# Performance work log

Hardware: AMD Instinct MI355X
Metric: run time of the kernel (lower is better)

## Reference

```python
import jax, jax.numpy as jnp
import numpy as np

N = 500_000
EMB = 256
G = 4096


def setup_inputs() -> dict:
    key = jax.random.key(0)
    k1, k2, k3, k4, k5, k6 = jax.random.split(key, 6)
    values = jax.random.normal(k1, (N, EMB), dtype=jnp.float32)
    indices = jnp.sort(jax.random.randint(k2, (N,), 0, G, dtype=jnp.int64))
    # Linear params (torch Linear: y = x @ W.T + b); stored pre-transposed.
    lim_g = 1.0 / np.sqrt(EMB)
    gate_w = jax.random.uniform(k3, (EMB, 1), jnp.float32, -lim_g, lim_g)
    gate_b = jax.random.uniform(k4, (1,), jnp.float32, -lim_g, lim_g)
    attn_w = jax.random.uniform(k5, (EMB, EMB), jnp.float32, -lim_g, lim_g)
    attn_b = jax.random.uniform(k6, (EMB,), jnp.float32, -lim_g, lim_g)
    return {
        "values": values,
        "indices": indices,
        "num_graphs": G,
        "gate_w": gate_w,
        "gate_b": gate_b,
        "attn_w": attn_w,
        "attn_b": attn_b,
    }


def reference(values, indices, num_graphs, gate_w, gate_b, attn_w, attn_b):
    # Gate scores: [N, 1]
    s = values @ gate_w + gate_b
    # Segmented softmax over nodes grouped by graph id (numerically stable).
    seg_max = jax.ops.segment_max(s, indices, num_segments=num_graphs)  # [G, 1]
    e = jnp.exp(s - seg_max[indices])                                   # [N, 1]
    denom = jax.ops.segment_sum(e, indices, num_segments=num_graphs)   # [G, 1]
    w = e / denom[indices]                                              # [N, 1]
    # Attention projection and weighted segment sum.
    a = values @ attn_w + attn_b                                        # [N, EMB]
    out = jax.ops.segment_sum(w * a, indices, num_segments=num_graphs)  # [G, EMB]
    return out
```

## Files before the change

### kernel.cpp

```cpp
#include <hip/hip_runtime.h>
#include <math.h>

#define EMB 256

__global__ void k_bounds(const int* __restrict__ idx, int* __restrict__ seg_start,
                         int n, int g) {
    int t = blockIdx.x * blockDim.x + threadIdx.x;
    if (t > g) return;
    int lo = 0, hi = n;
    while (lo < hi) {
        int mid = (lo + hi) >> 1;
        if (idx[mid] < t) lo = mid + 1; else hi = mid;
    }
    seg_start[t] = lo;
}

__global__ void __launch_bounds__(256) k_fused(const float* __restrict__ vals,
                                               const float* __restrict__ gate_w,
                                               const float* __restrict__ gate_b,
                                               const int* __restrict__ seg_start,
                                               float* __restrict__ wvec) {
    const int g = blockIdx.x;
    const int start = seg_start[g], end = seg_start[g + 1];
    const int cnt = end - start;
    const int t = threadIdx.x;
    const int lane = t & 63, w = t >> 6;

    __shared__ float m_s[4], d_s[4];
    __shared__ float partial[4][EMB];

    if (cnt <= 0) {
        wvec[(size_t)g * EMB + t] = 0.0f;
        return;
    }

    const float4 gw = *reinterpret_cast<const float4*>(gate_w + lane * 4);
    const float  gb = gate_b[0];

    float m = -INFINITY, d = 0.0f;
    float4 acc = {0.f, 0.f, 0.f, 0.f};

    for (int j = start + w; j < end; j += 4) {
        float4 v = *reinterpret_cast<const float4*>(vals + (size_t)j * EMB + lane * 4);
        float si = v.x * gw.x + v.y * gw.y + v.z * gw.z + v.w * gw.w;
        #pragma unroll
        for (int o = 1; o < 64; o <<= 1) si += __shfl_xor(si, o);
        si += gb;
        if (si > m) {
            const float scale = expf(m - si);
            d *= scale;
            acc.x *= scale; acc.y *= scale; acc.z *= scale; acc.w *= scale;
            m = si;
        }
        const float p = expf(si - m);
        d += p;
        acc.x += p * v.x; acc.y += p * v.y; acc.z += p * v.z; acc.w += p * v.w;
    }

    if (lane == 0) m_s[w] = m;
    __syncthreads();
    const float M = fmaxf(fmaxf(m_s[0], m_s[1]), fmaxf(m_s[2], m_s[3]));
    const float f = expf(m - M);
    if (lane == 0) d_s[w] = d * f;
    acc.x *= f; acc.y *= f; acc.z *= f; acc.w *= f;
    *reinterpret_cast<float4*>(&partial[w][lane * 4]) = acc;
    __syncthreads();
    const float dt = d_s[0] + d_s[1] + d_s[2] + d_s[3];
    wvec[(size_t)g * EMB + t] =
        (partial[0][t] + partial[1][t] + partial[2][t] + partial[3][t]) / dt;
}

__global__ void __launch_bounds__(256) k_gemm(const float* __restrict__ A,
                                              const float* __restrict__ W,
                                              const float* __restrict__ bias,
                                              const int* __restrict__ seg_start,
                                              float* __restrict__ out) {
    __shared__ float A_s[64][68];
    __shared__ float B_s[64][64];
    const int bid = blockIdx.x;
    const int row0 = (bid >> 2) * 64;
    const int col0 = (bid & 3) * 64;
    const int t = threadIdx.x;
    const int ty = t >> 4, tx = t & 15;

    float acc[4][4] = {};

    for (int kc = 0; kc < EMB; kc += 64) {
        #pragma unroll
        for (int l = t; l < 64 * 16; l += 256) {
            int r = l >> 4, c4 = (l & 15) << 2;
            float4 v = *reinterpret_cast<const float4*>(
                A + (size_t)(row0 + r) * EMB + kc + c4);
            *reinterpret_cast<float4*>(&A_s[r][c4]) = v;
        }
        #pragma unroll
        for (int l = t; l < 64 * 16; l += 256) {
            int r = l >> 4, c4 = (l & 15) << 2;
            *reinterpret_cast<float4*>(&B_s[r][c4]) =
                *reinterpret_cast<const float4*>(
                    W + (size_t)(kc + r) * EMB + col0 + c4);
        }
        __syncthreads();

        #pragma unroll
        for (int k = 0; k < 64; k += 4) {
            float a[4][4], b[4][4];
            #pragma unroll
            for (int i = 0; i < 4; ++i)
                *reinterpret_cast<float4*>(a[i]) =
                    *reinterpret_cast<const float4*>(&A_s[ty * 4 + i][k]);
            #pragma unroll
            for (int kk = 0; kk < 4; ++kk)
                *reinterpret_cast<float4*>(b[kk]) =
                    *reinterpret_cast<const float4*>(&B_s[k + kk][tx * 4]);
            #pragma unroll
            for (int i = 0; i < 4; ++i)
                #pragma unroll
                for (int kk = 0; kk < 4; ++kk)
                    #pragma unroll
                    for (int j = 0; j < 4; ++j)
                        acc[i][j] += a[i][kk] * b[kk][j];
        }
        __syncthreads();
    }

    const float4 b4 = *reinterpret_cast<const float4*>(bias + col0 + tx * 4);
    #pragma unroll
    for (int i = 0; i < 4; ++i) {
        const int r = row0 + ty * 4 + i;
        const float bs = (seg_start[r + 1] - seg_start[r]) > 0 ? 1.0f : 0.0f;
        float4 o;
        o.x = acc[i][0] + bs * b4.x;
        o.y = acc[i][1] + bs * b4.y;
        o.z = acc[i][2] + bs * b4.z;
        o.w = acc[i][3] + bs * b4.w;
        *reinterpret_cast<float4*>(out + (size_t)r * EMB + col0 + tx * 4) = o;
    }
}

extern "C" void kernel_launch(void* const* d_in, const int* in_sizes, int n_in,
                              void* d_out, int out_size, void* d_ws, size_t ws_size,
                              hipStream_t stream) {
    const float* vals   = (const float*)d_in[0];
    const int*   idx    = (const int*)d_in[1];
    const float* gate_w = (const float*)d_in[3];
    const float* gate_b = (const float*)d_in[4];
    const float* attn_w = (const float*)d_in[5];
    const float* attn_b = (const float*)d_in[6];
    float* out = (float*)d_out;

    const int n = in_sizes[1];
    const int g = out_size / EMB;

    int*   seg_start = (int*)d_ws;
    float* wvec = (float*)((char*)d_ws + (((g + 1) * 4 + 15) & ~15));

    k_bounds<<<(g + 256) / 256, 256, 0, stream>>>(idx, seg_start, n, g);
    k_fused<<<g, 256, 0, stream>>>(vals, gate_w, gate_b, seg_start, wvec);
    k_gemm<<<(g / 64) * 4, 256, 0, stream>>>(wvec, attn_w, attn_b, seg_start, out);
}
```

Baseline: 131.6 us.

## Process four rows per wave iteration with nontemporal loads and fast exp

Each wave in the fused segment-softmax kernel now handles four consecutive rows per iteration instead of one. It issues four vector loads at once, as nontemporal loads, and runs the four warp reductions interleaved. The online-softmax rescale is done once per group of four using the group maximum, and `expf` is replaced with `__expf`. The aim is more memory-level parallelism and less serialized shuffle and exp latency on a bandwidth-bound stream. The cost is extra tail-masking logic, higher register use and slightly lower exp precision.

```diff
diff --git a/kernel.cpp b/kernel.cpp
--- a/kernel.cpp
+++ b/kernel.cpp
@@ -2,6 +2,8 @@
 #include <math.h>
 
 #define EMB 256
+
+typedef float f32x4 __attribute__((ext_vector_type(4)));
 
 __global__ void k_bounds(const int* __restrict__ idx, int* __restrict__ seg_start,
                          int n, int g) {
@@ -34,36 +36,67 @@
         return;
     }
 
-    const float4 gw = *reinterpret_cast<const float4*>(gate_w + lane * 4);
-    const float  gb = gate_b[0];
+    const f32x4 gw = *reinterpret_cast<const f32x4*>(gate_w + lane * 4);
+    const float gb = gate_b[0];
 
     float m = -INFINITY, d = 0.0f;
-    float4 acc = {0.f, 0.f, 0.f, 0.f};
+    f32x4 acc = {0.f, 0.f, 0.f, 0.f};
 
-    for (int j = start + w; j < end; j += 4) {
-        float4 v = *reinterpret_cast<const float4*>(vals + (size_t)j * EMB + lane * 4);
-        float si = v.x * gw.x + v.y * gw.y + v.z * gw.z + v.w * gw.w;
+    for (int j = start + w * 4; j < end; j += 16) {
+        f32x4 v0 = {0,0,0,0}, v1 = {0,0,0,0}, v2 = {0,0,0,0}, v3 = {0,0,0,0};
+        const float* p0 = vals + (size_t)j * EMB + lane * 4;
+        if (j + 3 < end) {
+            v0 = __builtin_nontemporal_load(reinterpret_cast<const f32x4*>(p0));
+            v1 = __builtin_nontemporal_load(reinterpret_cast<const f32x4*>(p0 + EMB));
+            v2 = __builtin_nontemporal_load(reinterpret_cast<const f32x4*>(p0 + 2 * EMB));
+            v3 = __builtin_nontemporal_load(reinterpret_cast<const f32x4*>(p0 + 3 * EMB));
+        } else {
+            v0 = __builtin_nontemporal_load(reinterpret_cast<const f32x4*>(p0));
+            if (j + 1 < end) v1 = __builtin_nontemporal_load(reinterpret_cast<const f32x4*>(p0 + EMB));
+            if (j + 2 < end) v2 = __builtin_nontemporal_load(reinterpret_cast<const f32x4*>(p0 + 2 * EMB));
+        }
+
+        float s0 = v0.x * gw.x + v0.y * gw.y + v0.z * gw.z + v0.w * gw.w;
+        float s1 = v1.x * gw.x + v1.y * gw.y + v1.z * gw.z + v1.w * gw.w;
+        float s2 = v2.x * gw.x + v2.y * gw.y + v2.z * gw.z + v2.w * gw.w;
+        float s3 = v3.x * gw.x + v3.y * gw.y + v3.z * gw.z + v3.w * gw.w;
         #pragma unroll
-        for (int o = 1; o < 64; o <<= 1) si += __shfl_xor(si, o);
-        si += gb;
-        if (si > m) {
-            const float scale = expf(m - si);
-            d *= scale;
-            acc.x *= scale; acc.y *= scale; acc.z *= scale; acc.w *= scale;
-            m = si;
+        for (int o = 1; o < 64; o <<= 1) {
+            s0 += __shfl_xor(s0, o);
+            s1 += __shfl_xor(s1, o);
+            s2 += __shfl_xor(s2, o);
+            s3 += __shfl_xor(s3, o);
         }
-        const float p = expf(si - m);
-        d += p;
-        acc.x += p * v.x; acc.y += p * v.y; acc.z += p * v.z; acc.w += p * v.w;
+        s0 += gb; s1 += gb; s2 += gb; s3 += gb;
+        if (j + 3 >= end) {
+            if (j + 1 >= end) s1 = -INFINITY;
+            if (j + 2 >= end) s2 = -INFINITY;
+            s3 = -INFINITY;
+        }
+
+        const float mx = fmaxf(fmaxf(s0, s1), fmaxf(s2, s3));
+        if (mx > m) {
+            const float sc = __expf(m - mx);
+            d *= sc;
+            acc.x *= sc; acc.y *= sc; acc.z *= sc; acc.w *= sc;
+            m = mx;
+        }
+        const float e0 = __expf(s0 - m), e1 = __expf(s1 - m);
+        const float e2 = __expf(s2 - m), e3 = __expf(s3 - m);
+        d += (e0 + e1) + (e2 + e3);
+        acc.x += e0 * v0.x + e1 * v1.x + e2 * v2.x + e3 * v3.x;
+        acc.y += e0 * v0.y + e1 * v1.y + e2 * v2.y + e3 * v3.y;
+        acc.z += e0 * v0.z + e1 * v1.z + e2 * v2.z + e3 * v3.z;
+        acc.w += e0 * v0.w + e1 * v1.w + e2 * v2.w + e3 * v3.w;
     }
 
     if (lane == 0) m_s[w] = m;
     __syncthreads();
     const float M = fmaxf(fmaxf(m_s[0], m_s[1]), fmaxf(m_s[2], m_s[3]));
-    const float f = expf(m - M);
+    const float f = __expf(m - M);
     if (lane == 0) d_s[w] = d * f;
     acc.x *= f; acc.y *= f; acc.z *= f; acc.w *= f;
-    *reinterpret_cast<float4*>(&partial[w][lane * 4]) = acc;
+    *reinterpret_cast<f32x4*>(&partial[w][lane * 4]) = acc;
     __syncthreads();
     const float dt = d_s[0] + d_s[1] + d_s[2] + d_s[3];
     wvec[(size_t)g * EMB + t] =
```

New measurement: 110.4 us. -16.1%, faster.
